# Kernel optimization log

Hardware: AMD Instinct MI355X
Metric: run time of the kernel (lower is better)

## Reference

```python
import jax, jax.numpy as jnp
import numpy as np

N_NODES = 100000
N_EDGES = 1600000
D_IN = 128
D_HID = 128
N_CLASSES = 8


def setup_inputs() -> dict:
    key = jax.random.key(0)
    ks = jax.random.split(key, 8)
    x = jax.random.normal(ks[0], (N_NODES, D_IN), dtype=jnp.float32)
    edge_index = jax.random.randint(ks[1], (2, N_EDGES), 0, N_NODES, dtype=jnp.int32)
    # Glorot-ish init for weights, zeros for biases (PyG GCNConv default)
    W1 = jax.random.normal(ks[2], (D_IN, D_HID), dtype=jnp.float32) / np.sqrt(D_IN)
    b1 = jnp.zeros((D_HID,), dtype=jnp.float32)
    W2 = jax.random.normal(ks[3], (D_HID, D_HID), dtype=jnp.float32) / np.sqrt(D_HID)
    b2 = jnp.zeros((D_HID,), dtype=jnp.float32)
    Wout = jax.random.normal(ks[4], (D_HID, N_CLASSES), dtype=jnp.float32) / np.sqrt(D_HID)
    bout = jnp.zeros((N_CLASSES,), dtype=jnp.float32)
    return {"x": x, "edge_index": edge_index, "W1": W1, "b1": b1,
            "W2": W2, "b2": b2, "Wout": Wout, "bout": bout}


def _gcn_conv(h, src, dst, norm, W, b, n_nodes):
    # h: [N, d_in]; src/dst: [E+N] (with self-loops); norm: [E+N]
    h = h @ W                                   # [N, d_out]
    msg = h[src] * norm[:, None]                # gather + edge-wise scale
    agg = jax.ops.segment_sum(msg, dst, num_segments=n_nodes)  # scatter-add
    return agg + b


def reference(x, edge_index, W1, b1, W2, b2, Wout, bout):
    n = x.shape[0]
    loops = jnp.arange(n, dtype=edge_index.dtype)
    src = jnp.concatenate([edge_index[0], loops])   # [E+N]
    dst = jnp.concatenate([edge_index[1], loops])   # [E+N]
    # symmetric normalization D^-1/2 (A+I) D^-1/2
    deg = jax.ops.segment_sum(jnp.ones_like(src, dtype=x.dtype), dst, num_segments=n)
    dinv = jnp.where(deg > 0, jax.lax.rsqrt(deg), 0.0)
    norm = dinv[src] * dinv[dst]                    # [E+N]

    h = _gcn_conv(x, src, dst, norm, W1, b1, n)
    h = jax.nn.relu(h)  # dropout is identity in eval mode
    h = _gcn_conv(h, src, dst, norm, W2, b2, n)
    h = jax.nn.relu(h)
    return jax.nn.softmax(h @ Wout + bout, axis=1)  # [N, 8]
```

## Files before the change

kernel.cpp:

```cpp
#include <hip/hip_runtime.h>
#include <hip/hip_fp16.h>

#define NN 100000
#define NE 1600000
#define D 128
#define NC 8
#define NBUCK 391
#define BCAP 6144
#define CHUNK 16384
#define NBLK_SC ((NE + CHUNK - 1) / CHUNK)

typedef _Float16 half8 __attribute__((ext_vector_type(8)));
typedef float f32x4 __attribute__((ext_vector_type(4)));

__global__ __launch_bounds__(256) void k_prep(const float* __restrict__ W1,
                                              __half* __restrict__ wt1,
                                              const float* __restrict__ W2,
                                              __half* __restrict__ wt2,
                                              const int* __restrict__ dst,
                                              int* __restrict__ cnt, int E) {
    const int t = threadIdx.x;
    if (blockIdx.x < 2) {
        const float* W = blockIdx.x ? W2 : W1;
        __half* wt = blockIdx.x ? wt2 : wt1;
        for (int i = t; i < D * D; i += 256) {
            int k = i >> 7, c = i & 127;
            wt[c * D + k] = __float2half(W[i]);
        }
        return;
    }
    int e0 = (blockIdx.x - 2) * 1024 + t * 4;
    if (e0 < E) {
        int4 d4 = *(const int4*)&dst[e0];
        atomicAdd(&cnt[d4.x], 1);
        atomicAdd(&cnt[d4.y], 1);
        atomicAdd(&cnt[d4.z], 1);
        atomicAdd(&cnt[d4.w], 1);
    }
}

template <bool F32IN>
__device__ __forceinline__ void gemm_body(const void* __restrict__ Ain,
                                          const __half* __restrict__ wt,
                                          const int* __restrict__ cnt,
                                          __half* __restrict__ hout, int gb) {
    const int tid = threadIdx.x;
    const int lane = tid & 63;
    const int wave = tid >> 6;
    const int wr = wave >> 1, wc = wave & 1;
    const int row0 = gb * 32 + wr * 16;
    const int arow = row0 + (lane & 15);
    const int kg = lane >> 4;

    half8 afrag[4];
    if constexpr (F32IN) {
        const float* A = (const float*)Ain;
#pragma unroll
        for (int s = 0; s < 4; ++s) {
            const float* p = &A[(size_t)arow * D + s * 32 + kg * 8];
            float4 f0 = *(const float4*)p;
            float4 f1 = *(const float4*)(p + 4);
            half8 a;
            a[0] = (_Float16)f0.x; a[1] = (_Float16)f0.y;
            a[2] = (_Float16)f0.z; a[3] = (_Float16)f0.w;
            a[4] = (_Float16)f1.x; a[5] = (_Float16)f1.y;
            a[6] = (_Float16)f1.z; a[7] = (_Float16)f1.w;
            afrag[s] = a;
        }
    } else {
        const __half* A = (const __half*)Ain;
#pragma unroll
        for (int s = 0; s < 4; ++s)
            afrag[s] = *(const half8*)&A[(size_t)arow * D + s * 32 + kg * 8];
    }

    f32x4 acc[4] = {};
    const int colbase = wc * 64;
#pragma unroll
    for (int c = 0; c < 4; ++c) {
        const int col = colbase + c * 16 + (lane & 15);
#pragma unroll
        for (int s = 0; s < 4; ++s) {
            half8 b = *(const half8*)&wt[col * D + s * 32 + kg * 8];
            acc[c] = __builtin_amdgcn_mfma_f32_16x16x32_f16(afrag[s], b, acc[c], 0, 0, 0);
        }
    }

#pragma unroll
    for (int r = 0; r < 4; ++r) {
        const int row = row0 + kg * 4 + r;
        const float dv = rsqrtf((float)(cnt[row] + 1));
#pragma unroll
        for (int c = 0; c < 4; ++c) {
            const int col = colbase + c * 16 + (lane & 15);
            hout[(size_t)row * D + col] = __float2half(acc[c][r] * dv);
        }
    }
}

__global__ __launch_bounds__(256) void k_work(const int* __restrict__ src,
                                              const int* __restrict__ dst,
                                              int* __restrict__ bcursor,
                                              int* __restrict__ staged,
                                              const float* __restrict__ x,
                                              const __half* __restrict__ wt1,
                                              const int* __restrict__ cnt,
                                              __half* __restrict__ hout, int E) {
    if (blockIdx.x < NBLK_SC) {
        __shared__ int h[NBUCK];
        __shared__ int cur[NBUCK];
        const int t = threadIdx.x;
        for (int i = t; i < NBUCK; i += 256) h[i] = 0;
        __syncthreads();
        const int base0 = blockIdx.x * CHUNK;
#pragma unroll
        for (int i = 0; i < CHUNK / 1024; ++i) {
            int e = base0 + i * 1024 + t * 4;
            if (e < E) {
                int4 d4 = *(const int4*)&dst[e];
                atomicAdd(&h[d4.x >> 8], 1);
                atomicAdd(&h[d4.y >> 8], 1);
                atomicAdd(&h[d4.z >> 8], 1);
                atomicAdd(&h[d4.w >> 8], 1);
            }
        }
        __syncthreads();
        for (int i = t; i < NBUCK; i += 256) {
            int c = h[i];
            cur[i] = c ? (i * BCAP + atomicAdd(&bcursor[i], c)) : 0;
        }
        __syncthreads();
#pragma unroll
        for (int i = 0; i < CHUNK / 1024; ++i) {
            int e = base0 + i * 1024 + t * 4;
            if (e < E) {
                int4 d4 = *(const int4*)&dst[e];
                int4 s4 = *(const int4*)&src[e];
                int p;
                p = atomicAdd(&cur[d4.x >> 8], 1); staged[p] = s4.x * 256 + (d4.x & 255);
                p = atomicAdd(&cur[d4.y >> 8], 1); staged[p] = s4.y * 256 + (d4.y & 255);
                p = atomicAdd(&cur[d4.z >> 8], 1); staged[p] = s4.z * 256 + (d4.z & 255);
                p = atomicAdd(&cur[d4.w >> 8], 1); staged[p] = s4.w * 256 + (d4.w & 255);
            }
        }
        return;
    }
    gemm_body<true>(x, wt1, cnt, hout, blockIdx.x - NBLK_SC);
}

__global__ __launch_bounds__(256) void k_bfill(const int* __restrict__ staged,
                                               const int* __restrict__ bcursor,
                                               const int* __restrict__ cnt,
                                               int* __restrict__ rowstart,
                                               int* __restrict__ csr) {
    const int b = blockIdx.x;
    const int t = threadIdx.x;
    const int bs = b * BCAP;
    const int be = bs + bcursor[b];
    __shared__ int ls[256];
    __shared__ int sd[256];
    __shared__ int lc[256];
    const int node = (b << 8) + t;
    int v = (node < NN) ? cnt[node] : 0;
    sd[t] = v;
    __syncthreads();
    for (int off = 1; off < 256; off <<= 1) {
        int y = (t >= off) ? sd[t - off] : 0;
        __syncthreads();
        sd[t] += y;
        __syncthreads();
    }
    int ex = sd[t] - v;
    ls[t] = bs + ex;
    if (node < NN) rowstart[node] = bs + ex;
    lc[t] = 0;
    __syncthreads();
    for (int i = bs + t; i < be; i += 256) {
        int e = staged[i];
        int li = e & 255;
        int p = atomicAdd(&lc[li], 1);
        csr[ls[li] + p] = e >> 8;
    }
}

__global__ __launch_bounds__(256) void k_gemm2(const __half* __restrict__ A,
                                               const __half* __restrict__ wt,
                                               const int* __restrict__ cnt,
                                               __half* __restrict__ hout) {
    gemm_body<false>(A, wt, cnt, hout, blockIdx.x);
}

__device__ inline void add8h(float* acc, float4 raw) {
    const __half2* hp = (const __half2*)&raw;
#pragma unroll
    for (int q = 0; q < 4; ++q) {
        float2 f = __half22float2(hp[q]);
        acc[2 * q] += f.x;
        acc[2 * q + 1] += f.y;
    }
}

__global__ __launch_bounds__(256) void k_agg(const __half* __restrict__ hs,
                                             const int* __restrict__ rowstart,
                                             const int* __restrict__ cnt,
                                             const int* __restrict__ csr_src,
                                             const float* __restrict__ bias,
                                             __half* __restrict__ hout) {
    const int node = blockIdx.x * 4 + (threadIdx.x >> 6);
    const int lane = threadIdx.x & 63;
    const int g = lane >> 4;
    const int f8 = (lane & 15) << 3;

    float acc[8] = {};
    if (g == 0) add8h(acc, *(const float4*)&hs[(size_t)node * D + f8]);

    const int c = cnt[node];
    const int* __restrict__ cl = csr_src + rowstart[node];

    int t = g;
    while (t < c) {
        float4 v[8];
#pragma unroll
        for (int i = 0; i < 8; ++i) {
            int tt = t + 4 * i;
            if (tt < c) {
                int s = cl[tt];
                v[i] = *(const float4*)&hs[(size_t)s * D + f8];
            }
        }
#pragma unroll
        for (int i = 0; i < 8; ++i) {
            int tt = t + 4 * i;
            if (tt < c) add8h(acc, v[i]);
        }
        t += 32;
    }

#pragma unroll
    for (int q = 0; q < 8; ++q) {
        acc[q] += __shfl_xor(acc[q], 16);
        acc[q] += __shfl_xor(acc[q], 32);
    }

    if (g == 0) {
        const float dv = rsqrtf((float)(c + 1));
        float r[8];
#pragma unroll
        for (int q = 0; q < 8; ++q) r[q] = fmaxf(fmaf(dv, acc[q], bias[f8 + q]), 0.f);
        union { float4 f; __half2 h[4]; } u;
#pragma unroll
        for (int q = 0; q < 4; ++q) u.h[q] = __floats2half2_rn(r[2 * q], r[2 * q + 1]);
        *(float4*)&hout[(size_t)node * D + f8] = u.f;
    }
}

__global__ void k_out(const __half* __restrict__ h, const float* __restrict__ Wout,
                      const float* __restrict__ bout, float* __restrict__ out, int n) {
    __shared__ float ws[D * NC];
    int tid = threadIdx.x;
    for (int i = tid; i < D * NC; i += 256) ws[i] = Wout[i];
    __syncthreads();
    int node = blockIdx.x * 32 + (tid >> 3);
    int c = tid & 7;
    if (node >= n) return;
    float acc = bout[c];
    const __half* hrow = &h[(size_t)node * D];
#pragma unroll
    for (int k8 = 0; k8 < 16; ++k8) {
        float4 raw = *(const float4*)&hrow[k8 * 8];
        const __half2* hp = (const __half2*)&raw;
#pragma unroll
        for (int q = 0; q < 4; ++q) {
            float2 f = __half22float2(hp[q]);
            int k = k8 * 8 + 2 * q;
            acc += f.x * ws[k * NC + c] + f.y * ws[(k + 1) * NC + c];
        }
    }
    float m = acc;
#pragma unroll
    for (int off = 1; off < 8; off <<= 1) m = fmaxf(m, __shfl_xor(m, off));
    float e = __expf(acc - m);
    float ssum = e;
#pragma unroll
    for (int off = 1; off < 8; off <<= 1) ssum += __shfl_xor(ssum, off);
    out[(size_t)node * NC + c] = e / ssum;
}

extern "C" void kernel_launch(void* const* d_in, const int* in_sizes, int n_in,
                              void* d_out, int out_size, void* d_ws, size_t ws_size,
                              hipStream_t stream) {
    const float* x    = (const float*)d_in[0];
    const int*   ei   = (const int*)d_in[1];
    const float* W1   = (const float*)d_in[2];
    const float* b1   = (const float*)d_in[3];
    const float* W2   = (const float*)d_in[4];
    const float* b2   = (const float*)d_in[5];
    const float* Wout = (const float*)d_in[6];
    const float* bout = (const float*)d_in[7];
    float* out = (float*)d_out;

    size_t off = 0;
    char* base = (char*)d_ws;
    auto alloc = [&](size_t bytes) -> void* {
        void* p = base + off;
        off += (bytes + 255) & ~(size_t)255;
        return p;
    };
    int*    cnt      = (int*)alloc((size_t)NN * 4);
    int*    bcursor  = (int*)alloc((size_t)NBUCK * 4);
    int*    rowstart = (int*)alloc((size_t)NN * 4);
    int*    csr      = (int*)alloc((size_t)NBUCK * BCAP * 4);
    __half* wt1      = (__half*)alloc((size_t)D * D * 2);
    __half* wt2      = (__half*)alloc((size_t)D * D * 2);
    __half* h16a     = (__half*)alloc((size_t)NN * D * 2);
    __half* h16f     = (__half*)alloc((size_t)NN * D * 2);
    __half* h16b     = (__half*)alloc((size_t)NN * D * 2);
    int*    staged   = (int*)alloc((size_t)NBUCK * BCAP * 4);
    if (off > ws_size) return;

    const int* src = ei;
    const int* dst = ei + NE;

    hipMemsetAsync(cnt, 0, ((size_t)NN * 4 + 255 & ~(size_t)255) + (size_t)NBUCK * 4,
                   stream);

    k_prep<<<2 + (NE / 4 + 255) / 256, 256, 0, stream>>>(W1, wt1, W2, wt2, dst, cnt, NE);

    k_work<<<NBLK_SC + NN / 32, 256, 0, stream>>>(src, dst, bcursor, staged,
                                                  x, wt1, cnt, h16a, NE);

    k_bfill<<<NBUCK, 256, 0, stream>>>(staged, bcursor, cnt, rowstart, csr);

    int agg_grid = NN / 4;
    k_agg<<<agg_grid, 256, 0, stream>>>(h16a, rowstart, cnt, csr, b1, h16f);
    k_gemm2<<<NN / 32, 256, 0, stream>>>(h16f, wt2, cnt, h16a);
    k_agg<<<agg_grid, 256, 0, stream>>>(h16a, rowstart, cnt, csr, b2, h16b);
    k_out<<<(NN + 31) / 32, 256, 0, stream>>>(h16b, Wout, bout, out, NN);
}
```

Before: 325.1 us.

## Derive degrees from bucketed edges and apply source norm in aggregation

```diff
diff --git a/kernel.cpp b/kernel.cpp
--- a/kernel.cpp
+++ b/kernel.cpp
@@ -13,36 +13,19 @@
 typedef _Float16 half8 __attribute__((ext_vector_type(8)));
 typedef float f32x4 __attribute__((ext_vector_type(4)));
 
-__global__ __launch_bounds__(256) void k_prep(const float* __restrict__ W1,
-                                              __half* __restrict__ wt1,
-                                              const float* __restrict__ W2,
-                                              __half* __restrict__ wt2,
-                                              const int* __restrict__ dst,
-                                              int* __restrict__ cnt, int E) {
-    const int t = threadIdx.x;
-    if (blockIdx.x < 2) {
-        const float* W = blockIdx.x ? W2 : W1;
-        __half* wt = blockIdx.x ? wt2 : wt1;
-        for (int i = t; i < D * D; i += 256) {
-            int k = i >> 7, c = i & 127;
-            wt[c * D + k] = __float2half(W[i]);
-        }
-        return;
-    }
-    int e0 = (blockIdx.x - 2) * 1024 + t * 4;
-    if (e0 < E) {
-        int4 d4 = *(const int4*)&dst[e0];
-        atomicAdd(&cnt[d4.x], 1);
-        atomicAdd(&cnt[d4.y], 1);
-        atomicAdd(&cnt[d4.z], 1);
-        atomicAdd(&cnt[d4.w], 1);
+__global__ void k_cvtw(const float* __restrict__ W1, __half* __restrict__ wt1,
+                       const float* __restrict__ W2, __half* __restrict__ wt2) {
+    const float* W = blockIdx.x ? W2 : W1;
+    __half* wt = blockIdx.x ? wt2 : wt1;
+    for (int i = threadIdx.x; i < D * D; i += 256) {
+        int k = i >> 7, c = i & 127;
+        wt[c * D + k] = __float2half(W[i]);
     }
 }
 
 template <bool F32IN>
 __device__ __forceinline__ void gemm_body(const void* __restrict__ Ain,
                                           const __half* __restrict__ wt,
-                                          const int* __restrict__ cnt,
                                           __half* __restrict__ hout, int gb) {
     const int tid = threadIdx.x;
     const int lane = tid & 63;
@@ -89,11 +72,10 @@
 #pragma unroll
     for (int r = 0; r < 4; ++r) {
         const int row = row0 + kg * 4 + r;
-        const float dv = rsqrtf((float)(cnt[row] + 1));
 #pragma unroll
         for (int c = 0; c < 4; ++c) {
             const int col = colbase + c * 16 + (lane & 15);
-            hout[(size_t)row * D + col] = __float2half(acc[c][r] * dv);
+            hout[(size_t)row * D + col] = __float2half(acc[c][r]);
         }
     }
 }
@@ -104,7 +86,6 @@
                                               int* __restrict__ staged,
                                               const float* __restrict__ x,
                                               const __half* __restrict__ wt1,
-                                              const int* __restrict__ cnt,
                                               __half* __restrict__ hout, int E) {
     if (blockIdx.x < NBLK_SC) {
         __shared__ int h[NBUCK];
@@ -145,23 +126,29 @@
         }
         return;
     }
-    gemm_body<true>(x, wt1, cnt, hout, blockIdx.x - NBLK_SC);
+    gemm_body<true>(x, wt1, hout, blockIdx.x - NBLK_SC);
 }
 
 __global__ __launch_bounds__(256) void k_bfill(const int* __restrict__ staged,
                                                const int* __restrict__ bcursor,
-                                               const int* __restrict__ cnt,
                                                int* __restrict__ rowstart,
+                                               int* __restrict__ cnt,
+                                               float* __restrict__ dinv,
                                                int* __restrict__ csr) {
     const int b = blockIdx.x;
     const int t = threadIdx.x;
     const int bs = b * BCAP;
     const int be = bs + bcursor[b];
+    __shared__ int lc[256];
     __shared__ int ls[256];
     __shared__ int sd[256];
-    __shared__ int lc[256];
-    const int node = (b << 8) + t;
-    int v = (node < NN) ? cnt[node] : 0;
+    lc[t] = 0;
+    __syncthreads();
+    for (int i = bs + t; i < be; i += 256) {
+        atomicAdd(&lc[staged[i] & 255], 1);
+    }
+    __syncthreads();
+    int v = lc[t];
     sd[t] = v;
     __syncthreads();
     for (int off = 1; off < 256; off <<= 1) {
@@ -172,7 +159,12 @@
     }
     int ex = sd[t] - v;
     ls[t] = bs + ex;
-    if (node < NN) rowstart[node] = bs + ex;
+    int node = (b << 8) + t;
+    if (node < NN) {
+        rowstart[node] = bs + ex;
+        cnt[node] = v;
+        dinv[node] = rsqrtf((float)(v + 1));
+    }
     lc[t] = 0;
     __syncthreads();
     for (int i = bs + t; i < be; i += 256) {
@@ -185,18 +177,17 @@
 
 __global__ __launch_bounds__(256) void k_gemm2(const __half* __restrict__ A,
                                                const __half* __restrict__ wt,
-                                               const int* __restrict__ cnt,
                                                __half* __restrict__ hout) {
-    gemm_body<false>(A, wt, cnt, hout, blockIdx.x);
-}
-
-__device__ inline void add8h(float* acc, float4 raw) {
+    gemm_body<false>(A, wt, hout, blockIdx.x);
+}
+
+__device__ inline void fma8h(float* acc, float4 raw, float s) {
     const __half2* hp = (const __half2*)&raw;
 #pragma unroll
     for (int q = 0; q < 4; ++q) {
         float2 f = __half22float2(hp[q]);
-        acc[2 * q] += f.x;
-        acc[2 * q + 1] += f.y;
+        acc[2 * q] = fmaf(s, f.x, acc[2 * q]);
+        acc[2 * q + 1] = fmaf(s, f.y, acc[2 * q + 1]);
     }
 }
 
@@ -204,6 +195,7 @@
                                              const int* __restrict__ rowstart,
                                              const int* __restrict__ cnt,
                                              const int* __restrict__ csr_src,
+                                             const float* __restrict__ dinv,
                                              const float* __restrict__ bias,
                                              __half* __restrict__ hout) {
     const int node = blockIdx.x * 4 + (threadIdx.x >> 6);
@@ -211,8 +203,10 @@
     const int g = lane >> 4;
     const int f8 = (lane & 15) << 3;
 
+    const float dvn = dinv[node];
     float acc[8] = {};
-    if (g == 0) add8h(acc, *(const float4*)&hs[(size_t)node * D + f8]);
+    if (g == 0)
+        fma8h(acc, *(const float4*)&hs[(size_t)node * D + f8], dvn);
 
     const int c = cnt[node];
     const int* __restrict__ cl = csr_src + rowstart[node];
@@ -220,18 +214,20 @@
     int t = g;
     while (t < c) {
         float4 v[8];
+        float dv8[8];
 #pragma unroll
         for (int i = 0; i < 8; ++i) {
             int tt = t + 4 * i;
             if (tt < c) {
                 int s = cl[tt];
                 v[i] = *(const float4*)&hs[(size_t)s * D + f8];
+                dv8[i] = dinv[s];
             }
         }
 #pragma unroll
         for (int i = 0; i < 8; ++i) {
             int tt = t + 4 * i;
-            if (tt < c) add8h(acc, v[i]);
+            if (tt < c) fma8h(acc, v[i], dv8[i]);
         }
         t += 32;
     }
@@ -243,10 +239,9 @@
     }
 
     if (g == 0) {
-        const float dv = rsqrtf((float)(c + 1));
         float r[8];
 #pragma unroll
-        for (int q = 0; q < 8; ++q) r[q] = fmaxf(fmaf(dv, acc[q], bias[f8 + q]), 0.f);
+        for (int q = 0; q < 8; ++q) r[q] = fmaxf(fmaf(dvn, acc[q], bias[f8 + q]), 0.f);
         union { float4 f; __half2 h[4]; } u;
 #pragma unroll
         for (int q = 0; q < 4; ++q) u.h[q] = __floats2half2_rn(r[2 * q], r[2 * q + 1]);
@@ -307,9 +302,10 @@
         return p;
     };
     int*    cnt      = (int*)alloc((size_t)NN * 4);
+    int*    rowstart = (int*)alloc((size_t)NN * 4);
     int*    bcursor  = (int*)alloc((size_t)NBUCK * 4);
-    int*    rowstart = (int*)alloc((size_t)NN * 4);
     int*    csr      = (int*)alloc((size_t)NBUCK * BCAP * 4);
+    float*  dinv     = (float*)alloc((size_t)NN * 4);
     __half* wt1      = (__half*)alloc((size_t)D * D * 2);
     __half* wt2      = (__half*)alloc((size_t)D * D * 2);
     __half* h16a     = (__half*)alloc((size_t)NN * D * 2);
@@ -321,19 +317,18 @@
     const int* src = ei;
     const int* dst = ei + NE;
 
-    hipMemsetAsync(cnt, 0, ((size_t)NN * 4 + 255 & ~(size_t)255) + (size_t)NBUCK * 4,
-                   stream);
-
-    k_prep<<<2 + (NE / 4 + 255) / 256, 256, 0, stream>>>(W1, wt1, W2, wt2, dst, cnt, NE);
+    hipMemsetAsync(bcursor, 0, (size_t)NBUCK * 4, stream);
+
+    k_cvtw<<<2, 256, 0, stream>>>(W1, wt1, W2, wt2);
 
     k_work<<<NBLK_SC + NN / 32, 256, 0, stream>>>(src, dst, bcursor, staged,
-                                                  x, wt1, cnt, h16a, NE);
-
-    k_bfill<<<NBUCK, 256, 0, stream>>>(staged, bcursor, cnt, rowstart, csr);
+                                                  x, wt1, h16a, NE);
+
+    k_bfill<<<NBUCK, 256, 0, stream>>>(staged, bcursor, rowstart, cnt, dinv, csr);
 
     int agg_grid = NN / 4;
-    k_agg<<<agg_grid, 256, 0, stream>>>(h16a, rowstart, cnt, csr, b1, h16f);
-    k_gemm2<<<NN / 32, 256, 0, stream>>>(h16f, wt2, cnt, h16a);
-    k_agg<<<agg_grid, 256, 0, stream>>>(h16a, rowstart, cnt, csr, b2, h16b);
+    k_agg<<<agg_grid, 256, 0, stream>>>(h16a, rowstart, cnt, csr, dinv, b1, h16f);
+    k_gemm2<<<NN / 32, 256, 0, stream>>>(h16f, wt2, h16a);
+    k_agg<<<agg_grid, 256, 0, stream>>>(h16a, rowstart, cnt, csr, dinv, b2, h16b);
     k_out<<<(NN + 31) / 32, 256, 0, stream>>>(h16b, Wout, bout, out, NN);
 }
```

Result: faster. 280.7 us (-13.7%).
